# Kernel tuning notes

Measured on AMD Instinct MI355X. Metric: run time of the kernel, lower is better.

The kernel has to match this reference:

```python
import jax, jax.numpy as jnp
import numpy as np

B = 2048      # number of ragged rows
R = 10        # row size: 1 anchor + 1 pos + 8 negatives
D = 1024      # embedding dim
ALPHA = 1.0
BETA = 0.5
TEMP = 0.05


def setup_inputs() -> dict:
    key = jax.random.key(0)
    k1, k2 = jax.random.split(key)
    embeddings = jax.random.normal(k1, (B * R, D), dtype=jnp.float32)
    scores = jax.random.normal(k2, (B * (R - 1),), dtype=jnp.float32)
    row_sizes = jnp.full((B,), R, dtype=jnp.int64)
    return {"embeddings": embeddings, "scores": scores, "row_sizes": row_sizes}


def _l2norm(x, eps=1e-12):
    return x / jnp.maximum(jnp.linalg.norm(x, axis=-1, keepdims=True), eps)


def reference(embeddings, scores, row_sizes):
    b = row_sizes.shape[0]
    r = embeddings.shape[0] // b           # uniform row size
    d = embeddings.shape[1]
    emb = embeddings.reshape(b, r, d)
    anchor = emb[:, 0]                      # [B, D]
    pos = emb[:, 1]                         # [B, D]
    negs = emb[:, 2:]                       # [B, R-2, D]

    # per-row cosine similarities: anchor vs pos, anchor vs each neg
    a_n = _l2norm(anchor)
    pos_score = jnp.sum(a_n * _l2norm(pos), axis=-1)                 # [B]
    neg_scores = jnp.einsum('bd,bkd->bk', a_n, _l2norm(negs))        # [B, R-2]
    row_scores = jnp.concatenate([pos_score[:, None], neg_scores], axis=1)  # [B, R-1]

    # KLDivLoss(reduction='batchmean') per row: sum(t*(log t - log p)) / (R-1)
    log_p = jax.nn.log_softmax(row_scores, axis=1)
    ce = jax.nn.softmax(scores.reshape(b, r - 1), axis=1)
    kl_per_row = jnp.sum(jax.scipy.special.xlogy(ce, ce) - ce * log_p, axis=1) / (r - 1)
    loss = BETA * jnp.mean(kl_per_row)

    # single InfoNCE over the whole batch: targets = [pos; all negs]
    targets = jnp.concatenate([pos, negs.reshape(b * (r - 2), d)], axis=0)  # [B*(R-1), D]
    sim = (a_n @ _l2norm(targets).T) / TEMP                                 # [B, B*(R-1)]
    logz = jax.nn.logsumexp(sim, axis=1)
    diag = sim[jnp.arange(b), jnp.arange(b)]
    ce_loss = jnp.mean(logz - diag)
    loss = loss + ALPHA * ce_loss
    return loss
```

## Files before the change

kernel.cpp:

```cpp
#include <hip/hip_runtime.h>
#include <hip/hip_bf16.h>
#include <stdint.h>

#define NB 2048
#define NR 10
#define ND 1024
#define NTGT (NB * (NR - 1))
#define INV_TEMP 20.0f

#define BM 128
#define BN 256
#define BK 64
#define NKT (ND / BK)
#define TM_TILES (NB / BM)
#define TN_TILES (NTGT / BN)

typedef __attribute__((ext_vector_type(4))) float floatx4;
typedef __attribute__((ext_vector_type(2))) long longx2;

#define BAR()    asm volatile("s_barrier" ::: "memory")
#define VMCNT0() asm volatile("s_waitcnt vmcnt(0)" ::: "memory")
#define VMCNT3() asm volatile("s_waitcnt vmcnt(3)" ::: "memory")

__device__ __forceinline__ void async16(const void* g, void* l) {
  __builtin_amdgcn_global_load_lds(
      (const __attribute__((address_space(1))) unsigned int*)g,
      (__attribute__((address_space(3))) unsigned int*)l,
      16, 0, 0);
}

__global__ __launch_bounds__(256) void prep_kernel(
    const float* __restrict__ emb, const float* __restrict__ scores,
    unsigned char* __restrict__ A8, unsigned char* __restrict__ T8,
    float* __restrict__ pos_score, float* __restrict__ kl_out,
    float* __restrict__ sumexp) {
  int b = blockIdx.x;
  int tid = threadIdx.x;
  int wid = tid >> 6, lane = tid & 63;
  const float* base = emb + (size_t)b * NR * ND;

  if (tid == 32) sumexp[b] = 0.0f;

  float4 v[NR];
  float ss[NR], dt[NR - 1];
#pragma unroll
  for (int r = 0; r < NR; ++r) {
    v[r] = reinterpret_cast<const float4*>(base + (size_t)r * ND)[tid];
    ss[r] = v[r].x * v[r].x + v[r].y * v[r].y + v[r].z * v[r].z + v[r].w * v[r].w;
  }
#pragma unroll
  for (int t = 0; t < NR - 1; ++t)
    dt[t] = v[0].x * v[t + 1].x + v[0].y * v[t + 1].y + v[0].z * v[t + 1].z +
            v[0].w * v[t + 1].w;

#pragma unroll
  for (int off = 32; off; off >>= 1) {
#pragma unroll
    for (int r = 0; r < NR; ++r) ss[r] += __shfl_xor(ss[r], off, 64);
#pragma unroll
    for (int t = 0; t < NR - 1; ++t) dt[t] += __shfl_xor(dt[t], off, 64);
  }
  __shared__ float red[4][2 * NR - 1];
  if (lane == 0) {
#pragma unroll
    for (int r = 0; r < NR; ++r) red[wid][r] = ss[r];
#pragma unroll
    for (int t = 0; t < NR - 1; ++t) red[wid][NR + t] = dt[t];
  }
  __syncthreads();

  float inv[NR];
#pragma unroll
  for (int r = 0; r < NR; ++r) {
    float s = red[0][r] + red[1][r] + red[2][r] + red[3][r];
    inv[r] = 1.0f / fmaxf(sqrtf(s), 1e-12f);
  }

#pragma unroll
  for (int r = 0; r < NR; ++r) {
    unsigned char* dst;
    if (r == 0)      dst = A8 + (size_t)b * ND;
    else if (r == 1) dst = T8 + (size_t)b * ND;
    else             dst = T8 + (size_t)(NB + b * 8 + (r - 2)) * ND;
    int p = 0;
    p = __builtin_amdgcn_cvt_pk_fp8_f32(v[r].x * inv[r], v[r].y * inv[r], p, false);
    p = __builtin_amdgcn_cvt_pk_fp8_f32(v[r].z * inv[r], v[r].w * inv[r], p, true);
    reinterpret_cast<int*>(dst)[tid] = p;
  }

  if (tid == 0) {
    float rs[NR - 1];
#pragma unroll
    for (int t = 0; t < NR - 1; ++t) {
      float d = red[0][NR + t] + red[1][NR + t] + red[2][NR + t] + red[3][NR + t];
      rs[t] = d * inv[0] * inv[t + 1];
    }
    float sc[NR - 1], ms = -1e30f;
#pragma unroll
    for (int k = 0; k < NR - 1; ++k) { sc[k] = scores[b * (NR - 1) + k]; ms = fmaxf(ms, sc[k]); }
    float se = 0.f;
#pragma unroll
    for (int k = 0; k < NR - 1; ++k) { sc[k] = expf(sc[k] - ms); se += sc[k]; }
    float mr = -1e30f;
#pragma unroll
    for (int k = 0; k < NR - 1; ++k) mr = fmaxf(mr, rs[k]);
    float sr = 0.f;
#pragma unroll
    for (int k = 0; k < NR - 1; ++k) sr += expf(rs[k] - mr);
    float lz = logf(sr) + mr;
    float kl = 0.f;
#pragma unroll
    for (int k = 0; k < NR - 1; ++k) {
      float ce = sc[k] / se;
      kl += ce * logf(ce) - ce * (rs[k] - lz);
    }
    kl_out[b] = kl / (float)(NR - 1);
    pos_score[b] = rs[0];
  }
}


__device__ __forceinline__ void stage_A8(const unsigned char* __restrict__ gtile,
                                         unsigned char* lds, int k0, int tid) {
  int lrow = tid >> 2;
  int u = (tid & 3) ^ ((lrow >> 1) & 3);
  const unsigned char* src = gtile + (size_t)lrow * ND + k0 + u * 16;
  unsigned char* dst = lds + (tid & ~63) * 16;
  async16(src, dst);
}

__device__ __forceinline__ void stage_B8(const unsigned char* __restrict__ gtile,
                                         unsigned char* lds, int k0, int tid) {
#pragma unroll
  for (int r = 0; r < 2; ++r) {
    int slot = r * 512 + tid;
    int lrow = slot >> 2;
    int u = (slot & 3) ^ ((lrow >> 1) & 3);
    const unsigned char* src = gtile + (size_t)lrow * ND + k0 + u * 16;
    unsigned char* dst = lds + (r * 512 + (tid & ~63)) * 16;
    async16(src, dst);
  }
}

__device__ __forceinline__ longx2 frag8(const unsigned char* lds, int row, int lq) {
  int byte = row * 64 + ((lq * 16) ^ (((row >> 1) & 3) << 4));
  return *reinterpret_cast<const longx2*>(lds + byte);
}

__global__ __launch_bounds__(512, 4) void gemm_lse_kernel(
    const unsigned char* __restrict__ A, const unsigned char* __restrict__ T,
    float* __restrict__ sumexp) {
  __shared__ unsigned char smem[3 * (BM + BN) * BK];

  int bid = blockIdx.x;
  int xcd = bid & 7;
  int j = bid >> 3;
  int tn = xcd * 9 + (j >> 4);
  int tm = j & 15;

  int tid = threadIdx.x;
  int wid = tid >> 6, lane = tid & 63;
  int wm = wid >> 2, wn = wid & 3;
  int lrow = lane & 15, lq = lane >> 4;

  const unsigned char* Ag = A + (size_t)tm * BM * ND;
  const unsigned char* Tg = T + (size_t)tn * BN * ND;

  floatx4 acc[4][4] = {};

  unsigned char* bufA0 = smem;
  unsigned char* bufB0 = smem + BM * BK;
  unsigned char* bufA1 = smem + (BM + BN) * BK;
  unsigned char* bufB1 = bufA1 + BM * BK;
  unsigned char* bufA2 = smem + 2 * (BM + BN) * BK;
  unsigned char* bufB2 = bufA2 + BM * BK;

  stage_A8(Ag, bufA0, 0, tid);
  stage_B8(Tg, bufB0, 0, tid);
  stage_A8(Ag, bufA1, BK, tid);
  stage_B8(Tg, bufB1, BK, tid);
  VMCNT3();
  BAR();

  const unsigned char* Acur = bufA0;  const unsigned char* Bcur = bufB0;
  unsigned char* Anxt = bufA1;        unsigned char* Bnxt = bufB1;
  unsigned char* Afar = bufA2;        unsigned char* Bfar = bufB2;

  for (int s = 0; s < NKT; ++s) {
    const int kn = ((s + 2) & (NKT - 1)) * BK;
    stage_A8(Ag, Afar, kn, tid);
    stage_B8(Tg, Bfar, kn, tid);

    longx2 aF[4], bF[4];
#pragma unroll
    for (int m = 0; m < 4; ++m)
      aF[m] = frag8(Acur, wm * 64 + m * 16 + lrow, lq);
#pragma unroll
    for (int n = 0; n < 4; ++n)
      bF[n] = frag8(Bcur, wn * 64 + n * 16 + lrow, lq);

    __builtin_amdgcn_s_setprio(1);
#pragma unroll
    for (int m = 0; m < 4; ++m)
#pragma unroll
      for (int n = 0; n < 4; ++n) {
        acc[m][n] = __builtin_amdgcn_mfma_f32_16x16x32_fp8_fp8(aF[m].x, bF[n].x, acc[m][n], 0, 0, 0);
        acc[m][n] = __builtin_amdgcn_mfma_f32_16x16x32_fp8_fp8(aF[m].y, bF[n].y, acc[m][n], 0, 0, 0);
      }
    __builtin_amdgcn_s_setprio(0);

    VMCNT3();
    BAR();

    unsigned char* ta = (unsigned char*)Acur;  unsigned char* tb = (unsigned char*)Bcur;
    Acur = Anxt;  Bcur = Bnxt;
    Anxt = Afar;  Bnxt = Bfar;
    Afar = ta;    Bfar = tb;
  }

  VMCNT0();

#pragma unroll
  for (int m = 0; m < 4; ++m) {
#pragma unroll
    for (int j2 = 0; j2 < 4; ++j2) {
      float s = __expf(acc[m][0][j2] * INV_TEMP) + __expf(acc[m][1][j2] * INV_TEMP) +
                __expf(acc[m][2][j2] * INV_TEMP) + __expf(acc[m][3][j2] * INV_TEMP);
      s += __shfl_xor(s, 1, 64);
      s += __shfl_xor(s, 2, 64);
      s += __shfl_xor(s, 4, 64);
      s += __shfl_xor(s, 8, 64);
      if (lrow == 0) {
        int grow = tm * BM + wm * 64 + m * 16 + lq * 4 + j2;
        atomicAdd(&sumexp[grow], s);
      }
    }
  }
}

__global__ __launch_bounds__(256) void finalize_kernel(
    const float* __restrict__ sumexp, const float* __restrict__ pos_score,
    const float* __restrict__ kl, float* __restrict__ out) {
  int tid = threadIdx.x;
  float kls = 0.f, ces = 0.f;
  for (int i = tid; i < NB; i += 256) {
    kls += kl[i];
    ces += logf(sumexp[i]) - pos_score[i] * INV_TEMP;
  }
#pragma unroll
  for (int off = 32; off; off >>= 1) {
    kls += __shfl_xor(kls, off, 64);
    ces += __shfl_xor(ces, off, 64);
  }
  __shared__ float sk[4], se4[4];
  int wid = tid >> 6, lane = tid & 63;
  if (lane == 0) { sk[wid] = kls; se4[wid] = ces; }
  __syncthreads();
  if (tid == 0) {
    float k4 = sk[0] + sk[1] + sk[2] + sk[3];
    float e4 = se4[0] + se4[1] + se4[2] + se4[3];
    out[0] = 0.5f * (k4 / (float)NB) + 1.0f * (e4 / (float)NB);
  }
}

extern "C" void kernel_launch(void* const* d_in, const int* in_sizes, int n_in,
                              void* d_out, int out_size, void* d_ws, size_t ws_size,
                              hipStream_t stream) {
  const float* emb = (const float*)d_in[0];
  const float* scores = (const float*)d_in[1];
  float* out = (float*)d_out;

  char* ws = (char*)d_ws;
  size_t offA = 0;
  size_t offT = offA + (size_t)NB * ND;
  size_t offSum = offT + (size_t)NTGT * ND;
  size_t offPos = offSum + (size_t)NB * 4;
  size_t offKl = offPos + (size_t)NB * 4;

  unsigned char* A8 = (unsigned char*)(ws + offA);
  unsigned char* T8 = (unsigned char*)(ws + offT);
  float* sumexp = (float*)(ws + offSum);
  float* pos_score = (float*)(ws + offPos);
  float* kl = (float*)(ws + offKl);

  prep_kernel<<<NB, 256, 0, stream>>>(emb, scores, A8, T8, pos_score, kl, sumexp);
  gemm_lse_kernel<<<dim3(TM_TILES * TN_TILES), 512, 0, stream>>>(A8, T8, sumexp);
  finalize_kernel<<<1, 256, 0, stream>>>(sumexp, pos_score, kl, out);
}
```

Baseline: 85.87 us.

## Reshape GEMM tile to 256x192 and split A/B loading across wave groups

Changes the FP8 GEMM block tile from 128x256 to 256x192, so each wave computes a 128x48 sub-tile (8x3 MFMA fragments) instead of 64x64. Global-to-LDS staging is split so the first four waves load A and the last four load B, each with its own vmcnt wait. The grid remapping over XCDs is adjusted to the new tile counts. The goal is better operand reuse and fewer redundant loads per FLOP. The trade-off is more accumulator registers and a dropped occupancy hint, which may lower occupancy.

Measured after the change: 138.2 us. +60.9%, slower.

```diff
diff --git a/kernel.cpp b/kernel.cpp
--- a/kernel.cpp
+++ b/kernel.cpp
@@ -8,19 +8,19 @@
 #define NTGT (NB * (NR - 1))
 #define INV_TEMP 20.0f
 
-#define BM 128
-#define BN 256
+#define BM 256
+#define BN 192
 #define BK 64
 #define NKT (ND / BK)
 #define TM_TILES (NB / BM)
 #define TN_TILES (NTGT / BN)
+#define KTILE_BYTES ((BM + BN) * BK)
 
 typedef __attribute__((ext_vector_type(4))) float floatx4;
 typedef __attribute__((ext_vector_type(2))) long longx2;
 
 #define BAR()    asm volatile("s_barrier" ::: "memory")
 #define VMCNT0() asm volatile("s_waitcnt vmcnt(0)" ::: "memory")
-#define VMCNT3() asm volatile("s_waitcnt vmcnt(3)" ::: "memory")
 
 __device__ __forceinline__ void async16(const void* g, void* l) {
   __builtin_amdgcn_global_load_lds(
@@ -120,25 +120,31 @@
 }
 
 
-__device__ __forceinline__ void stage_A8(const unsigned char* __restrict__ gtile,
-                                         unsigned char* lds, int k0, int tid) {
-  int lrow = tid >> 2;
-  int u = (tid & 3) ^ ((lrow >> 1) & 3);
-  const unsigned char* src = gtile + (size_t)lrow * ND + k0 + u * 16;
-  unsigned char* dst = lds + (tid & ~63) * 16;
-  async16(src, dst);
-}
-
-__device__ __forceinline__ void stage_B8(const unsigned char* __restrict__ gtile,
-                                         unsigned char* lds, int k0, int tid) {
-#pragma unroll
-  for (int r = 0; r < 2; ++r) {
-    int slot = r * 512 + tid;
+__device__ __forceinline__ void stage_A(const unsigned char* __restrict__ gtile,
+                                        unsigned char* lds, int k0,
+                                        int wid, int lane) {
+  int li = wid * 64 + lane;
+#pragma unroll
+  for (int r = 0; r < 4; ++r) {
+    int slot = r * 256 + li;
     int lrow = slot >> 2;
     int u = (slot & 3) ^ ((lrow >> 1) & 3);
-    const unsigned char* src = gtile + (size_t)lrow * ND + k0 + u * 16;
-    unsigned char* dst = lds + (r * 512 + (tid & ~63)) * 16;
-    async16(src, dst);
+    async16(gtile + (size_t)lrow * ND + k0 + u * 16,
+            lds + (r * 256 + wid * 64) * 16);
+  }
+}
+
+__device__ __forceinline__ void stage_B(const unsigned char* __restrict__ gtile,
+                                        unsigned char* lds, int k0,
+                                        int wid4, int lane) {
+  int li = wid4 * 64 + lane;
+#pragma unroll
+  for (int r = 0; r < 3; ++r) {
+    int slot = r * 256 + li;
+    int lrow = slot >> 2;
+    int u = (slot & 3) ^ ((lrow >> 1) & 3);
+    async16(gtile + (size_t)lrow * ND + k0 + u * 16,
+            lds + (r * 256 + wid4 * 64) * 16);
   }
 }
 
@@ -147,91 +153,97 @@
   return *reinterpret_cast<const longx2*>(lds + byte);
 }
 
-__global__ __launch_bounds__(512, 4) void gemm_lse_kernel(
+__global__ __launch_bounds__(512) void gemm_lse_kernel(
     const unsigned char* __restrict__ A, const unsigned char* __restrict__ T,
     float* __restrict__ sumexp) {
-  __shared__ unsigned char smem[3 * (BM + BN) * BK];
+  __shared__ unsigned char smem[3 * KTILE_BYTES];
 
   int bid = blockIdx.x;
   int xcd = bid & 7;
   int j = bid >> 3;
-  int tn = xcd * 9 + (j >> 4);
-  int tm = j & 15;
+  int tn = xcd * 12 + (j >> 3);
+  int tm = j & 7;
 
   int tid = threadIdx.x;
   int wid = tid >> 6, lane = tid & 63;
   int wm = wid >> 2, wn = wid & 3;
   int lrow = lane & 15, lq = lane >> 4;
+  bool isA = (wid < 4);
 
   const unsigned char* Ag = A + (size_t)tm * BM * ND;
   const unsigned char* Tg = T + (size_t)tn * BN * ND;
 
-  floatx4 acc[4][4] = {};
-
-  unsigned char* bufA0 = smem;
-  unsigned char* bufB0 = smem + BM * BK;
-  unsigned char* bufA1 = smem + (BM + BN) * BK;
-  unsigned char* bufB1 = bufA1 + BM * BK;
-  unsigned char* bufA2 = smem + 2 * (BM + BN) * BK;
-  unsigned char* bufB2 = bufA2 + BM * BK;
-
-  stage_A8(Ag, bufA0, 0, tid);
-  stage_B8(Tg, bufB0, 0, tid);
-  stage_A8(Ag, bufA1, BK, tid);
-  stage_B8(Tg, bufB1, BK, tid);
-  VMCNT3();
+  floatx4 acc[8][3] = {};
+
+  unsigned char* bufA[3], * bufB[3];
+#pragma unroll
+  for (int i = 0; i < 3; ++i) {
+    bufA[i] = smem + i * KTILE_BYTES;
+    bufB[i] = bufA[i] + BM * BK;
+  }
+
+  if (isA) {
+    stage_A(Ag, bufA[0], 0, wid, lane);
+    stage_A(Ag, bufA[1], BK, wid, lane);
+    asm volatile("s_waitcnt vmcnt(4)" ::: "memory");
+  } else {
+    stage_B(Tg, bufB[0], 0, wid - 4, lane);
+    stage_B(Tg, bufB[1], BK, wid - 4, lane);
+    asm volatile("s_waitcnt vmcnt(3)" ::: "memory");
+  }
   BAR();
 
-  const unsigned char* Acur = bufA0;  const unsigned char* Bcur = bufB0;
-  unsigned char* Anxt = bufA1;        unsigned char* Bnxt = bufB1;
-  unsigned char* Afar = bufA2;        unsigned char* Bfar = bufB2;
+  const unsigned char* Acur = bufA[0];  const unsigned char* Bcur = bufB[0];
+  unsigned char* An = bufA[1];          unsigned char* Bn = bufB[1];
+  unsigned char* Af = bufA[2];          unsigned char* Bf = bufB[2];
 
   for (int s = 0; s < NKT; ++s) {
     const int kn = ((s + 2) & (NKT - 1)) * BK;
-    stage_A8(Ag, Afar, kn, tid);
-    stage_B8(Tg, Bfar, kn, tid);
-
-    longx2 aF[4], bF[4];
-#pragma unroll
-    for (int m = 0; m < 4; ++m)
-      aF[m] = frag8(Acur, wm * 64 + m * 16 + lrow, lq);
-#pragma unroll
-    for (int n = 0; n < 4; ++n)
-      bF[n] = frag8(Bcur, wn * 64 + n * 16 + lrow, lq);
+    if (isA) stage_A(Ag, Af, kn, wid, lane);
+    else     stage_B(Tg, Bf, kn, wid - 4, lane);
+
+    longx2 aF[8], bF[3];
+#pragma unroll
+    for (int m = 0; m < 8; ++m)
+      aF[m] = frag8(Acur, wm * 128 + m * 16 + lrow, lq);
+#pragma unroll
+    for (int n = 0; n < 3; ++n)
+      bF[n] = frag8(Bcur, wn * 48 + n * 16 + lrow, lq);
 
     __builtin_amdgcn_s_setprio(1);
 #pragma unroll
-    for (int m = 0; m < 4; ++m)
-#pragma unroll
-      for (int n = 0; n < 4; ++n) {
+    for (int m = 0; m < 8; ++m)
+#pragma unroll
+      for (int n = 0; n < 3; ++n) {
         acc[m][n] = __builtin_amdgcn_mfma_f32_16x16x32_fp8_fp8(aF[m].x, bF[n].x, acc[m][n], 0, 0, 0);
         acc[m][n] = __builtin_amdgcn_mfma_f32_16x16x32_fp8_fp8(aF[m].y, bF[n].y, acc[m][n], 0, 0, 0);
       }
     __builtin_amdgcn_s_setprio(0);
 
-    VMCNT3();
+    if (isA) { asm volatile("s_waitcnt vmcnt(4)" ::: "memory"); }
+    else     { asm volatile("s_waitcnt vmcnt(3)" ::: "memory"); }
     BAR();
 
     unsigned char* ta = (unsigned char*)Acur;  unsigned char* tb = (unsigned char*)Bcur;
-    Acur = Anxt;  Bcur = Bnxt;
-    Anxt = Afar;  Bnxt = Bfar;
-    Afar = ta;    Bfar = tb;
+    Acur = An;  Bcur = Bn;
+    An = Af;    Bn = Bf;
+    Af = ta;    Bf = tb;
   }
 
   VMCNT0();
 
 #pragma unroll
-  for (int m = 0; m < 4; ++m) {
+  for (int m = 0; m < 8; ++m) {
 #pragma unroll
     for (int j2 = 0; j2 < 4; ++j2) {
       float s = __expf(acc[m][0][j2] * INV_TEMP) + __expf(acc[m][1][j2] * INV_TEMP) +
-                __expf(acc[m][2][j2] * INV_TEMP) + __expf(acc[m][3][j2] * INV_TEMP);
+                __expf(acc[m][2][j2] * INV_TEMP);
       s += __shfl_xor(s, 1, 64);
       s += __shfl_xor(s, 2, 64);
       s += __shfl_xor(s, 4, 64);
       s += __shfl_xor(s, 8, 64);
       if (lrow == 0) {
-        int grow = tm * BM + wm * 64 + m * 16 + lq * 4 + j2;
+        int grow = tm * BM + wm * 128 + m * 16 + lq * 4 + j2;
         atomicAdd(&sumexp[grow], s);
       }
     }
```
